# Kernel tuning notes

Hardware: AMD Instinct MI355X
Metric: run time of the kernel (lower is better)

Reference implementation:

```python
import jax, jax.numpy as jnp
import numpy as np

DIM = 64   # flow dimension
HID = 8    # hidden_dim=[8]
B = 131072 # batch of samples


def setup_inputs() -> dict:
    key = jax.random.key(0)
    ks = jax.random.split(key, 6)
    L = DIM - 1  # number of per-dim MLPs (layers[0..L-1], layer l has fan-in l+1)
    lim = float(np.sqrt(0.5))
    x = jax.random.normal(ks[0], (B, DIM), jnp.float32)
    initial_param = jax.random.uniform(ks[1], (2,), jnp.float32, -lim, lim)
    # Ragged Linear(fan_in=l+1, 8) weights stacked into padded [L, HID, L];
    # entries beyond column l are masked to zero in reference().
    fan_in = np.arange(1, DIM).astype(np.float32)          # (L,)
    bnd1 = (1.0 / np.sqrt(fan_in))[:, None, None]          # torch Linear default init bound
    W1 = jax.random.uniform(ks[2], (L, HID, L), jnp.float32, -1.0, 1.0) * bnd1
    b1 = jax.random.uniform(ks[3], (L, HID), jnp.float32, -1.0, 1.0) * bnd1[:, :, 0]
    bnd2 = 1.0 / np.sqrt(HID)
    W2 = jax.random.uniform(ks[4], (L, 2, HID), jnp.float32, -bnd2, bnd2)
    b2 = jax.random.uniform(ks[5], (L, 2), jnp.float32, -bnd2, bnd2)
    return {"x": x, "initial_param": initial_param, "W1": W1, "b1": b1, "W2": W2, "b2": b2}


def reference(x, initial_param, W1, b1, W2, b2):
    B_, D = x.shape
    L = W1.shape[0]  # D - 1
    # mask[l, d] = 1 iff d <= l  ->  layer l sees exactly x[:, :l+1]
    mask = jnp.tril(jnp.ones((L, L), x.dtype))
    W1m = W1 * mask[:, None, :]
    # all dim-1 tiny MLPs fused into two batched contractions
    h = jnp.tanh(jnp.einsum('bd,lhd->blh', x[:, :L], W1m) + b1)   # [B, L, HID]
    out = jnp.einsum('blh,loh->blo', h, W2) + b2                   # [B, L, 2]
    mu0 = jnp.broadcast_to(initial_param[0], (B_, 1)).astype(x.dtype)
    al0 = jnp.broadcast_to(initial_param[1], (B_, 1)).astype(x.dtype)
    mu = jnp.concatenate([mu0, out[:, :, 0]], axis=1)              # [B, D]
    alpha = jnp.concatenate([al0, out[:, :, 1]], axis=1)           # [B, D]
    z = x * jnp.exp(alpha) + mu
    log_det = jnp.sum(alpha, axis=1)
    return z, log_det
```

## Files before the change

kernel.cpp:

```cpp
#include <hip/hip_runtime.h>


#define DIMS 64
#define TPB  1024
#define WAVES 16
#define SPW  16

typedef __attribute__((ext_vector_type(8))) short short8;
typedef __attribute__((ext_vector_type(4))) float f32x4;
typedef __attribute__((ext_vector_type(4))) unsigned int uint4v;
typedef unsigned short ushort_t;
typedef unsigned int uint_t;

#if __has_builtin(__builtin_amdgcn_exp2f)
#define YSCALE 2.8853900817779268f
#define EXPY(x) __builtin_amdgcn_exp2f(x)
#else
#define YSCALE 2.0f
#define EXPY(x) __expf(x)
#endif

#define A_OFF 0
#define B_OFF 16384
#define C_OFF 49152
#define D_OFF 53248
#define E_OFF 55296
#define WT_BYTES 55808
#define WT_CHUNKS (WT_BYTES / 16)
#define XZ_OFF WT_BYTES
#define LDS_BYTES (WT_BYTES + WAVES * SPW * DIMS * 4)
#define PREP_N (24576 + 1664)

__device__ __align__(16) unsigned char g_ws[WT_BYTES];

__device__ __forceinline__ uint_t pk2bf(float a, float b) {
#if __has_builtin(__builtin_amdgcn_cvt_pk_bf16_f32)
    typedef __attribute__((ext_vector_type(2))) __bf16 bf16x2;
    bf16x2 r = __builtin_amdgcn_cvt_pk_bf16_f32(a, b);
    return __builtin_bit_cast(uint_t, r);
#else
    uint_t ua = __float_as_uint(a); ua += 0x7FFFu + ((ua >> 16) & 1u);
    uint_t ub = __float_as_uint(b); ub += 0x7FFFu + ((ub >> 16) & 1u);
    return (ub & 0xFFFF0000u) | (ua >> 16);
#endif
}

__device__ __forceinline__ ushort_t f2bf(float f) {
    uint_t u = __float_as_uint(f);
    u += 0x7FFFu + ((u >> 16) & 1u);
    return (ushort_t)(u >> 16);
}

__device__ __forceinline__ int logrow(int p) {
    int n = p & 15;
    return (p >> 5) * 32 + (n >> 2) * 8 + ((p >> 4) & 1) * 4 + (n & 3);
}

__global__ void siaf_prep(const float* __restrict__ W1, const float* __restrict__ b1,
                          const float* __restrict__ W2, const float* __restrict__ b2) {
    ushort_t* __restrict__ ws_u = (ushort_t*)g_ws;
    int i = blockIdx.x * 256 + threadIdx.x;
    if (i < 8192) {
        int p = i >> 5, e = i & 31;
        int cp = e >> 3, j = e & 7;
        int k = ((cp ^ (p & 3)) << 3) | j;
        int L = logrow(p), l = L >> 3, h = L & 7;
        float v = (k <= l) ? W1[(l * 8 + h) * 63 + k] * YSCALE : 0.0f;
        ws_u[i] = f2bf(v);
    } else if (i < 24576) {
        int v_ = i - 8192;
        int p = 256 + (v_ >> 6), e = v_ & 63;
        int cp = e >> 3, j = e & 7;
        int k = ((cp ^ (p & 7)) << 3) | j;
        int L = logrow(p), l = L >> 3, h = L & 7;
        float v = (l < 63 && k <= l) ? W1[(l * 8 + h) * 63 + k] * YSCALE : 0.0f;
        ws_u[i] = f2bf(v);
    } else if (i < PREP_N) {
        int f = i - 24576;
        float* fws = (float*)(ws_u + 24576);
        float v = 0.0f;
        if (f < 1024) {
            int l = f >> 4, o = (f >> 3) & 1, h = f & 7;
            if (l < 63) v = W2[(l * 2 + o) * 8 + h];
        } else if (f < 1536) {
            int p = f - 1024;
            int L = logrow(p), l = L >> 3, h = L & 7;
            if (l < 63) v = b1[l * 8 + h] * YSCALE;
        } else {
            int j = f - 1536, l = j >> 1, o = j & 1;
            if (l < 63) v = b2[l * 2 + o];
        }
        fws[f] = v;
    }
}

__device__ __forceinline__ float th(float t) {
    float e = EXPY(t);
    float r = __builtin_amdgcn_rcpf(e + 1.0f);
    return fmaf(-2.0f, r, 1.0f);
}

__global__ __launch_bounds__(TPB, 4) void siaf_main(
        const float* __restrict__ x, const float* __restrict__ ip,
        float* __restrict__ out, int nB) {
    extern __shared__ unsigned char lds[];

    {
        const uint4* __restrict__ wsv = (const uint4*)g_ws;
        uint4* dst = (uint4*)lds;
        for (int c = threadIdx.x; c < WT_CHUNKS; c += TPB) dst[c] = wsv[c];
    }
    __syncthreads();

    const ushort_t* wA  = (const ushort_t*)(lds + A_OFF);
    const ushort_t* wB  = (const ushort_t*)(lds + B_OFF);
    const float*    w2f = (const float*)(lds + C_OFF);
    const float*    b1f = (const float*)(lds + D_OFF);
    const float*    b2f = (const float*)(lds + E_OFF);

    const int tid  = threadIdx.x;
    const int wv   = tid >> 6, lane = tid & 63;
    const int s16  = lane & 15, quad = lane >> 4;
    const int sbase = blockIdx.x * (WAVES * SPW) + wv * SPW;
    float* xzw = (float*)(lds + XZ_OFF) + wv * (SPW * DIMS);

    #pragma unroll
    for (int g = 0; g < 4; ++g) {
        const float4 v = ((const float4*)(x + (size_t)sbase * DIMS))[g * 64 + lane];
        const int s_loc = 4 * g + quad;
        const int pc = (s16 ^ s_loc) & 15;
        *(float4*)(xzw + s_loc * 64 + pc * 4) = v;
    }
    const float ip0 = ip[0], ip1 = ip[1];

    short8 bfr[2];
    #pragma unroll
    for (int kh = 0; kh < 2; ++kh) {
        const int c0 = kh * 8 + quad * 2;
        float4 va = *(const float4*)(xzw + s16 * 64 + ((c0 ^ s16) & 15) * 4);
        float4 vb = *(const float4*)(xzw + s16 * 64 + (((c0 + 1) ^ s16) & 15) * 4);
        uint4v u = {pk2bf(va.x, va.y), pk2bf(va.z, va.w),
                    pk2bf(vb.x, vb.y), pk2bf(vb.z, vb.w)};
        bfr[kh] = __builtin_bit_cast(short8, u);
    }

    float lsum = 0.0f;
    #pragma unroll
    for (int w = 0; w < 16; ++w) {
        short8 a00, a10, a01{}, a11{};
        if (w < 8) {
            const ushort_t* base = wA + (w * 32 + s16) * 32;
            const int pc = quad ^ (s16 & 3);
            a00 = *(const short8*)(base + pc * 8);
            a10 = *(const short8*)(base + 512 + pc * 8);
        } else {
            const ushort_t* base = wB + ((w - 8) * 32 + s16) * 64;
            const int pc = quad ^ (s16 & 7);
            a00 = *(const short8*)(base + pc * 8);
            a10 = *(const short8*)(base + 1024 + pc * 8);
            a01 = *(const short8*)(base + (pc ^ 4) * 8);
            a11 = *(const short8*)(base + 1024 + (pc ^ 4) * 8);
        }
        const float4 bi0 = *(const float4*)(b1f + w * 32 + quad * 4);
        const float4 bi1 = *(const float4*)(b1f + w * 32 + 16 + quad * 4);

        f32x4 aE = {bi0.x, bi0.y, bi0.z, bi0.w};
        f32x4 aO = {bi1.x, bi1.y, bi1.z, bi1.w};
        aE = __builtin_amdgcn_mfma_f32_16x16x32_bf16(a00, bfr[0], aE, 0, 0, 0);
        aO = __builtin_amdgcn_mfma_f32_16x16x32_bf16(a10, bfr[0], aO, 0, 0, 0);
        if (w >= 8) {
            aE = __builtin_amdgcn_mfma_f32_16x16x32_bf16(a01, bfr[1], aE, 0, 0, 0);
            aO = __builtin_amdgcn_mfma_f32_16x16x32_bf16(a11, bfr[1], aO, 0, 0, 0);
        }

        const float t0 = th(aE[0]), t1 = th(aE[1]), t2 = th(aE[2]), t3 = th(aE[3]);
        const float t4 = th(aO[0]), t5 = th(aO[1]), t6 = th(aO[2]), t7 = th(aO[3]);

        const int l = 4 * w + quad;
        const float4 m0 = *(const float4*)(w2f + l * 16);
        const float4 m1 = *(const float4*)(w2f + l * 16 + 4);
        const float4 a0 = *(const float4*)(w2f + l * 16 + 8);
        const float4 a1 = *(const float4*)(w2f + l * 16 + 12);
        const float2 bb = *(const float2*)(b2f + l * 2);

        float mu = bb.x;
        mu = fmaf(m0.x, t0, mu); mu = fmaf(m0.y, t1, mu);
        mu = fmaf(m0.z, t2, mu); mu = fmaf(m0.w, t3, mu);
        mu = fmaf(m1.x, t4, mu); mu = fmaf(m1.y, t5, mu);
        mu = fmaf(m1.z, t6, mu); mu = fmaf(m1.w, t7, mu);
        float al = bb.y;
        al = fmaf(a0.x, t0, al); al = fmaf(a0.y, t1, al);
        al = fmaf(a0.z, t2, al); al = fmaf(a0.w, t3, al);
        al = fmaf(a1.x, t4, al); al = fmaf(a1.y, t5, al);
        al = fmaf(a1.z, t6, al); al = fmaf(a1.w, t7, al);

        const bool pad = (l == 63);
        const float alB = pad ? ip1 : al;
        const float muB = pad ? ip0 : mu;
        const int d = pad ? 0 : (l + 1);
        float* pz = xzw + s16 * 64 + ((((d >> 2) ^ s16) & 15) << 2) + (d & 3);
        *pz = fmaf(*pz, __expf(alB), muB);
        lsum += alB;
    }

    #pragma unroll
    for (int g = 0; g < 4; ++g) {
        const int s_loc = 4 * g + quad;
        const int pc = (s16 ^ s_loc) & 15;
        const float4 v = *(const float4*)(xzw + s_loc * 64 + pc * 4);
        ((float4*)(out + (size_t)sbase * DIMS))[g * 64 + lane] = v;
    }

    {
        float v = lsum;
        int r1 = __builtin_amdgcn_ds_swizzle(__float_as_int(v), 0x401F);
        v += __int_as_float(r1);
        int r2 = __builtin_amdgcn_ds_bpermute((lane ^ 32) << 2, __float_as_int(v));
        v += __int_as_float(r2);
        if (quad == 0)
            out[(size_t)nB * DIMS + sbase + s16] = v;
    }
}

extern "C" void kernel_launch(void* const* d_in, const int* in_sizes, int n_in,
                              void* d_out, int out_size, void* d_ws, size_t ws_size,
                              hipStream_t stream) {
    const float* x  = (const float*)d_in[0];
    const float* ip = (const float*)d_in[1];
    const float* W1 = (const float*)d_in[2];
    const float* b1 = (const float*)d_in[3];
    const float* W2 = (const float*)d_in[4];
    const float* b2 = (const float*)d_in[5];
    float* out = (float*)d_out;
    (void)d_ws; (void)ws_size;

    const int nB = in_sizes[0] / DIMS;

    (void)hipFuncSetAttribute((const void*)siaf_main,
                              hipFuncAttributeMaxDynamicSharedMemorySize, LDS_BYTES);

    siaf_prep<<<(PREP_N + 255) / 256, 256, 0, stream>>>(W1, b1, W2, b2);
    siaf_main<<<nB / (WAVES * SPW), TPB, LDS_BYTES, stream>>>(x, ip, out, nB);
}
```

Measured before the change: 112.7 us.

## Overlap weight staging with x load and double-buffer per-step weight fragments

Moves the global-to-LDS weight copy after the x tile load so both global reads are in flight together, and drops one barrier before the x-to-bf16 conversion. Adds register double-buffering of MFMA A-fragments and bias loads so the next step's LDS reads are issued before the current step's MFMAs. It also splits the second-layer FMA chains into two accumulators for more ILP and uses a direct exp2 intrinsic for the final exp. This raises register pressure at 4 waves/EU occupancy and slightly changes rounding order.

```diff
diff --git a/kernel.cpp b/kernel.cpp
--- a/kernel.cpp
+++ b/kernel.cpp
@@ -15,10 +15,13 @@
 #if __has_builtin(__builtin_amdgcn_exp2f)
 #define YSCALE 2.8853900817779268f
 #define EXPY(x) __builtin_amdgcn_exp2f(x)
+#define EXP2F(x) __builtin_amdgcn_exp2f(x)
 #else
 #define YSCALE 2.0f
 #define EXPY(x) __expf(x)
+#define EXP2F(x) exp2f(x)
 #endif
+#define LOG2E 1.4426950408889634f
 
 #define A_OFF 0
 #define B_OFF 16384
@@ -105,19 +108,6 @@
         float* __restrict__ out, int nB) {
     extern __shared__ unsigned char lds[];
 
-    {
-        const uint4* __restrict__ wsv = (const uint4*)g_ws;
-        uint4* dst = (uint4*)lds;
-        for (int c = threadIdx.x; c < WT_CHUNKS; c += TPB) dst[c] = wsv[c];
-    }
-    __syncthreads();
-
-    const ushort_t* wA  = (const ushort_t*)(lds + A_OFF);
-    const ushort_t* wB  = (const ushort_t*)(lds + B_OFF);
-    const float*    w2f = (const float*)(lds + C_OFF);
-    const float*    b1f = (const float*)(lds + D_OFF);
-    const float*    b2f = (const float*)(lds + E_OFF);
-
     const int tid  = threadIdx.x;
     const int wv   = tid >> 6, lane = tid & 63;
     const int s16  = lane & 15, quad = lane >> 4;
@@ -132,6 +122,12 @@
         *(float4*)(xzw + s_loc * 64 + pc * 4) = v;
     }
     const float ip0 = ip[0], ip1 = ip[1];
+
+    {
+        const uint4* __restrict__ wsv = (const uint4*)g_ws;
+        uint4* dst = (uint4*)lds;
+        for (int c = tid; c < WT_CHUNKS; c += TPB) dst[c] = wsv[c];
+    }
 
     short8 bfr[2];
     #pragma unroll
@@ -144,10 +140,15 @@
         bfr[kh] = __builtin_bit_cast(short8, u);
     }
 
-    float lsum = 0.0f;
-    #pragma unroll
-    for (int w = 0; w < 16; ++w) {
-        short8 a00, a10, a01{}, a11{};
+    __syncthreads();
+
+    const ushort_t* wA  = (const ushort_t*)(lds + A_OFF);
+    const ushort_t* wB  = (const ushort_t*)(lds + B_OFF);
+    const float*    w2f = (const float*)(lds + C_OFF);
+    const float*    b1f = (const float*)(lds + D_OFF);
+    const float*    b2f = (const float*)(lds + E_OFF);
+
+    auto ldfr = [&](int w, short8& a00, short8& a10, short8& a01, short8& a11) {
         if (w < 8) {
             const ushort_t* base = wA + (w * 32 + s16) * 32;
             const int pc = quad ^ (s16 & 3);
@@ -161,20 +162,21 @@
             a01 = *(const short8*)(base + (pc ^ 4) * 8);
             a11 = *(const short8*)(base + 1024 + (pc ^ 4) * 8);
         }
-        const float4 bi0 = *(const float4*)(b1f + w * 32 + quad * 4);
-        const float4 bi1 = *(const float4*)(b1f + w * 32 + 16 + quad * 4);
-
-        f32x4 aE = {bi0.x, bi0.y, bi0.z, bi0.w};
-        f32x4 aO = {bi1.x, bi1.y, bi1.z, bi1.w};
-        aE = __builtin_amdgcn_mfma_f32_16x16x32_bf16(a00, bfr[0], aE, 0, 0, 0);
-        aO = __builtin_amdgcn_mfma_f32_16x16x32_bf16(a10, bfr[0], aO, 0, 0, 0);
-        if (w >= 8) {
-            aE = __builtin_amdgcn_mfma_f32_16x16x32_bf16(a01, bfr[1], aE, 0, 0, 0);
-            aO = __builtin_amdgcn_mfma_f32_16x16x32_bf16(a11, bfr[1], aO, 0, 0, 0);
-        }
-
-        const float t0 = th(aE[0]), t1 = th(aE[1]), t2 = th(aE[2]), t3 = th(aE[3]);
-        const float t4 = th(aO[0]), t5 = th(aO[1]), t6 = th(aO[2]), t7 = th(aO[3]);
+    };
+    auto ldbi = [&](int w, float4& bi0, float4& bi1) {
+        bi0 = *(const float4*)(b1f + w * 32 + quad * 4);
+        bi1 = *(const float4*)(b1f + w * 32 + 16 + quad * 4);
+    };
+
+    short8 A00[2], A10[2], A01[2] = {}, A11[2] = {};
+    float4 BI0[2], BI1[2];
+    ldfr(0, A00[0], A10[0], A01[0], A11[0]);
+    ldbi(0, BI0[0], BI1[0]);
+
+    float lsum = 0.0f;
+    #pragma unroll
+    for (int w = 0; w < 16; ++w) {
+        const int cur = w & 1, nxt = cur ^ 1;
 
         const int l = 4 * w + quad;
         const float4 m0 = *(const float4*)(w2f + l * 16);
@@ -183,23 +185,42 @@
         const float4 a1 = *(const float4*)(w2f + l * 16 + 12);
         const float2 bb = *(const float2*)(b2f + l * 2);
 
-        float mu = bb.x;
-        mu = fmaf(m0.x, t0, mu); mu = fmaf(m0.y, t1, mu);
-        mu = fmaf(m0.z, t2, mu); mu = fmaf(m0.w, t3, mu);
-        mu = fmaf(m1.x, t4, mu); mu = fmaf(m1.y, t5, mu);
-        mu = fmaf(m1.z, t6, mu); mu = fmaf(m1.w, t7, mu);
-        float al = bb.y;
-        al = fmaf(a0.x, t0, al); al = fmaf(a0.y, t1, al);
-        al = fmaf(a0.z, t2, al); al = fmaf(a0.w, t3, al);
-        al = fmaf(a1.x, t4, al); al = fmaf(a1.y, t5, al);
-        al = fmaf(a1.z, t6, al); al = fmaf(a1.w, t7, al);
+        if (w < 15) {
+            ldfr(w + 1, A00[nxt], A10[nxt], A01[nxt], A11[nxt]);
+            ldbi(w + 1, BI0[nxt], BI1[nxt]);
+        }
+
+        f32x4 aE = {BI0[cur].x, BI0[cur].y, BI0[cur].z, BI0[cur].w};
+        f32x4 aO = {BI1[cur].x, BI1[cur].y, BI1[cur].z, BI1[cur].w};
+        aE = __builtin_amdgcn_mfma_f32_16x16x32_bf16(A00[cur], bfr[0], aE, 0, 0, 0);
+        aO = __builtin_amdgcn_mfma_f32_16x16x32_bf16(A10[cur], bfr[0], aO, 0, 0, 0);
+        if (w >= 8) {
+            aE = __builtin_amdgcn_mfma_f32_16x16x32_bf16(A01[cur], bfr[1], aE, 0, 0, 0);
+            aO = __builtin_amdgcn_mfma_f32_16x16x32_bf16(A11[cur], bfr[1], aO, 0, 0, 0);
+        }
+
+        const float t0 = th(aE[0]), t1 = th(aE[1]), t2 = th(aE[2]), t3 = th(aE[3]);
+        const float t4 = th(aO[0]), t5 = th(aO[1]), t6 = th(aO[2]), t7 = th(aO[3]);
+
+        float mu0 = bb.x, mu1 = m1.x * t4;
+        mu0 = fmaf(m0.x, t0, mu0); mu1 = fmaf(m1.y, t5, mu1);
+        mu0 = fmaf(m0.y, t1, mu0); mu1 = fmaf(m1.z, t6, mu1);
+        mu0 = fmaf(m0.z, t2, mu0); mu1 = fmaf(m1.w, t7, mu1);
+        mu0 = fmaf(m0.w, t3, mu0);
+        const float mu = mu0 + mu1;
+        float al0 = bb.y, al1 = a1.x * t4;
+        al0 = fmaf(a0.x, t0, al0); al1 = fmaf(a1.y, t5, al1);
+        al0 = fmaf(a0.y, t1, al0); al1 = fmaf(a1.z, t6, al1);
+        al0 = fmaf(a0.z, t2, al0); al1 = fmaf(a1.w, t7, al1);
+        al0 = fmaf(a0.w, t3, al0);
+        const float al = al0 + al1;
 
         const bool pad = (l == 63);
         const float alB = pad ? ip1 : al;
         const float muB = pad ? ip0 : mu;
         const int d = pad ? 0 : (l + 1);
         float* pz = xzw + s16 * 64 + ((((d >> 2) ^ s16) & 15) << 2) + (d & 3);
-        *pz = fmaf(*pz, __expf(alB), muB);
+        *pz = fmaf(*pz, EXP2F(alB * LOG2E), muB);
         lsum += alB;
     }
 
```

After: 114.2 us. No clear change (+1.4%).
